# Performance work log

Measured on AMD Instinct MI355X. Metric: run time of the kernel, lower is better.

The kernel has to match this reference:

```python
import jax, jax.numpy as jnp
import numpy as np

NUM_GROUPS = 64
TOPK = 8
BLOCK_M = 128
NUM_TOKENS = 8192
HIDDEN = 4096


def _build_perm(flat_ids_np, num_groups, block_m):
    """Single-pass histogram + stable sort + per-expert padding.

    Returns sorted_token_ids (int64, [total_padded]) and m_indices (int32,
    [total_padded]) exactly matching the torch per-expert loop semantics:
    each expert's slot list padded to a multiple of block_m by repeating its
    last slot (or zeros for empty experts).
    Output length is data-dependent, so this runs on host numpy (concrete
    values), mirroring the original module whose output shape is also
    data-dependent.
    """
    n = flat_ids_np.shape[0]
    order = np.argsort(flat_ids_np, kind="stable")  # token slots grouped by expert
    counts = np.bincount(flat_ids_np, minlength=num_groups)
    padded = (counts + block_m - 1) // block_m * block_m
    in_starts = np.concatenate([[0], np.cumsum(counts)])
    out_starts = np.concatenate([[0], np.cumsum(padded)])
    total = int(out_starts[-1])
    sorted_token_ids = np.zeros(total, dtype=np.int64)
    m_indices = np.zeros(total, dtype=np.int32)
    for e in range(num_groups):  # fixed small expert count
        c, p, o = int(counts[e]), int(padded[e]), int(out_starts[e])
        m_indices[o:o + p] = e
        if c > 0:
            seg = order[int(in_starts[e]):int(in_starts[e]) + c]
            sorted_token_ids[o:o + c] = seg
            sorted_token_ids[o + c:o + p] = seg[-1]  # pad with last slot
        # empty expert: rows stay zero (matches torch.zeros branch)
    np.clip(sorted_token_ids, None, n - 1, out=sorted_token_ids)
    return sorted_token_ids, m_indices


def setup_inputs() -> dict:
    key = jax.random.key(0)
    k1, k2 = jax.random.split(key)
    hidden_states = jax.random.normal(k1, (NUM_TOKENS, HIDDEN), dtype=jnp.bfloat16)
    topk_ids = jax.random.randint(k2, (NUM_TOKENS, TOPK), 0, NUM_GROUPS, dtype=jnp.int32)
    return {"hidden_states": hidden_states, "topk_ids": topk_ids}


def reference(hidden_states, topk_ids):
    m, _ = hidden_states.shape
    num_flat = m * TOPK
    flat_ids = np.asarray(topk_ids).reshape(-1)
    sorted_token_ids_np, m_indices_np = _build_perm(flat_ids, NUM_GROUPS, BLOCK_M)
    sorted_token_ids = jnp.asarray(sorted_token_ids_np)
    m_indices = jnp.asarray(m_indices_np)
    # inverse permutation for later unpermute (stable argsort breaks pad ties deterministically)
    inv_perm = jnp.argsort(sorted_token_ids, stable=True)[:num_flat]
    source_token_idx = sorted_token_ids // TOPK  # expert-contiguous gather indices
    output = hidden_states[source_token_idx]     # [total_padded, HIDDEN] bf16 gather
    return output, m_indices, inv_perm
```

## Files before the change

kernel.cpp:

```cpp
#include <hip/hip_runtime.h>
#include <hip/hip_bf16.h>

#define NG 64
#define TOPK 8
#define BM 128
#define NSLOT 65536
#define HID 4096
#define NTOK 8192


__global__ __launch_bounds__(64) void init_k(int* ws) {
    int t = threadIdx.x;
    if (t < NG) { ws[t] = 0; ws[NG + t] = -1; }
}

__global__ void hist_k(const int* __restrict__ ids, int* __restrict__ ws) {
    __shared__ int h[NG];
    __shared__ int lm[NG];
    int t = threadIdx.x;
    if (t < NG) { h[t] = 0; lm[t] = -1; }
    __syncthreads();
    for (int i = blockIdx.x * blockDim.x + t; i < NSLOT; i += gridDim.x * blockDim.x) {
        int e = ids[i] & (NG - 1);
        atomicAdd(&h[e], 1);
        atomicMax(&lm[e], i);
    }
    __syncthreads();
    if (t < NG) {
        if (h[t]) atomicAdd(&ws[t], h[t]);
        atomicMax(&ws[NG + t], lm[t]);
    }
}

__global__ void scan_k(int* ws) {
    if (threadIdx.x == 0) {
        int acc = 0;
        for (int e = 0; e < NG; e++) {
            int c = ws[e];
            int p = (c + BM - 1) / BM * BM;
            ws[2 * NG + e] = p;
            ws[3 * NG + e] = acc;
            acc += p;
        }
        ws[256] = acc;
    }
}

__global__ __launch_bounds__(64) void rank_k(const int* __restrict__ ids,
                                             const int* __restrict__ ws,
                                             unsigned short* __restrict__ rank,
                                             float* __restrict__ out) {
    int e = blockIdx.x;
    int lane = threadIdx.x;
    int c = ws[e];
    int p = ws[2 * NG + e];
    int o = ws[3 * NG + e];
    int total = ws[256];

    if (c > 0) {
        int base_r = 0;
        for (int chunk = 0; chunk < NSLOT; chunk += 512) {
            int id[8];
#pragma unroll
            for (int u = 0; u < 8; u++) id[u] = ids[chunk + u * 64 + lane];
#pragma unroll
            for (int u = 0; u < 8; u++) {
                unsigned long long m = __ballot(id[u] == e);
                if (id[u] == e)
                    rank[chunk + u * 64 + lane] =
                        (unsigned short)(base_r + __popcll(m & ((1ULL << lane) - 1ULL)));
                base_r += __popcll(m);
            }
        }
    }
    float* m_out = out + (size_t)total * HID;
    float fe = (float)e;
    for (int t2 = lane; t2 < p; t2 += 64) {
        int idx = o + t2;
        if (idx >= 0 && idx < total) m_out[idx] = fe;
    }
}

__global__ void inv_k(const int* __restrict__ ids,
                      const int* __restrict__ ws,
                      const unsigned short* __restrict__ rank,
                      float* __restrict__ out) {
    __shared__ int s_last[NG], s_pad[NG];
    int t = threadIdx.x;
    if (t < NG) {
        s_last[t] = ws[NG + t];
        s_pad[t] = ws[2 * NG + t] - ws[t];
    }
    __syncthreads();
    int total = ws[256];
    float* inv_out = out + (size_t)total * (HID + 1);
    int i = blockIdx.x * blockDim.x + t;
    if (i >= NSLOT) return;
    int e = ids[i] & (NG - 1);
    int pos = ws[3 * NG + e] + (int)rank[i];
    int base = i;
#pragma unroll
    for (int f = 0; f < NG; f++) {
        int l = s_last[f];
        base += (l >= 0 && l < i) ? s_pad[f] : 0;
    }
    if (base >= 0 && base < NSLOT) inv_out[base] = (float)pos;
    if (i == s_last[e]) {
        int oc = ws[3 * NG + e] + ws[e];
        int pd = s_pad[e];
        for (int j = 0; j < pd; j++) {
            int idx = base + 1 + j;
            if (idx < 0 || idx >= NSLOT) break;
            inv_out[idx] = (float)(oc + j);
        }
    }
}

__global__ __launch_bounds__(256) void copy_k(const __hip_bfloat16* __restrict__ hs,
                                              const int* __restrict__ ids,
                                              const int* __restrict__ ws,
                                              const unsigned short* __restrict__ rank,
                                              float* __restrict__ out) {
    int b = blockIdx.x;
    int total = ws[256];
    int srcslot, dst;
    if (b < NSLOT) {
        int e = ids[b] & (NG - 1);
        srcslot = b;
        dst = ws[3 * NG + e] + (int)rank[b];
    } else {
        int q = b - NSLOT;
        int e = q >> 7;
        int j = q & 127;
        int c = ws[e];
        int p = ws[2 * NG + e];
        if (c + j >= p) return;
        srcslot = ws[NG + e];
        dst = ws[3 * NG + e] + c + j;
    }
    if (dst < 0 || dst >= total) return;
    int src = srcslot / TOPK;
    if (src < 0 || src >= NTOK) return;
    const uint4* s = (const uint4*)(hs + (size_t)src * HID);
    uint4* d = (uint4*)(out + (size_t)dst * HID);
    int t = threadIdx.x;
#pragma unroll
    for (int half = 0; half < 2; half++) {
        int v = half * 256 + t;
        uint4 w = s[v];
        uint4 o1, o2;
        o1.x = w.x << 16; o1.y = w.x & 0xFFFF0000u;
        o1.z = w.y << 16; o1.w = w.y & 0xFFFF0000u;
        o2.x = w.z << 16; o2.y = w.z & 0xFFFF0000u;
        o2.z = w.w << 16; o2.w = w.w & 0xFFFF0000u;
        d[2 * v] = o1;
        d[2 * v + 1] = o2;
    }
}

extern "C" void kernel_launch(void* const* d_in, const int* in_sizes, int n_in,
                              void* d_out, int out_size, void* d_ws, size_t ws_size,
                              hipStream_t stream) {
    const __hip_bfloat16* hs = (const __hip_bfloat16*)d_in[0];
    const int* ids = (const int*)d_in[1];
    float* out = (float*)d_out;

    int* ws = (int*)d_ws;
    unsigned short* rank = (unsigned short*)(ws + 512);

    hipLaunchKernelGGL(init_k, dim3(1), dim3(64), 0, stream, ws);
    hipLaunchKernelGGL(hist_k, dim3(64), dim3(256), 0, stream, ids, ws);
    hipLaunchKernelGGL(scan_k, dim3(1), dim3(64), 0, stream, ws);
    hipLaunchKernelGGL(rank_k, dim3(NG), dim3(64), 0, stream, ids, ws, rank, out);
    hipLaunchKernelGGL(inv_k, dim3(NSLOT / 256), dim3(256), 0, stream, ids, ws, rank, out);
    hipLaunchKernelGGL(copy_k, dim3(NSLOT + NG * BM), dim3(256), 0, stream,
                       hs, ids, ws, rank, out);
}
```

Baseline: 357.1 us.

## Segment histogram and rank per block to parallelize ranking; nontemporal output stores

Replaces the global atomic histogram with per-segment counts stored in the workspace, which removes the init kernel. The scan kernel now also builds per-segment prefix offsets for each expert, so ranking can be split across 4096 waves (expert × segment) instead of 64 waves that each scan all 65536 slots. The gather copy now uses nontemporal stores for the large fp32 output. The ranking kernel was a serial bottleneck; the cost is a larger workspace and a scan kernel with serial per-expert loops.

```diff
diff --git a/kernel.cpp b/kernel.cpp
--- a/kernel.cpp
+++ b/kernel.cpp
@@ -7,110 +7,117 @@
 #define NSLOT 65536
 #define HID 4096
 #define NTOK 8192
+#define NSEG 64
+
+typedef unsigned int v4u __attribute__((ext_vector_type(4)));
 
 
-__global__ __launch_bounds__(64) void init_k(int* ws) {
-    int t = threadIdx.x;
-    if (t < NG) { ws[t] = 0; ws[NG + t] = -1; }
-}
-
-__global__ void hist_k(const int* __restrict__ ids, int* __restrict__ ws) {
-    __shared__ int h[NG];
-    __shared__ int lm[NG];
-    int t = threadIdx.x;
+__global__ __launch_bounds__(256) void hist_k(const int* __restrict__ ids,
+                                              int* __restrict__ ws) {
+    __shared__ int h[NG], lm[NG];
+    int t = threadIdx.x, b = blockIdx.x;
     if (t < NG) { h[t] = 0; lm[t] = -1; }
     __syncthreads();
-    for (int i = blockIdx.x * blockDim.x + t; i < NSLOT; i += gridDim.x * blockDim.x) {
-        int e = ids[i] & (NG - 1);
+    int base = b * 1024;
+    for (int i = t; i < 1024; i += 256) {
+        int e = ids[base + i] & (NG - 1);
         atomicAdd(&h[e], 1);
-        atomicMax(&lm[e], i);
+        atomicMax(&lm[e], base + i);
     }
     __syncthreads();
     if (t < NG) {
-        if (h[t]) atomicAdd(&ws[t], h[t]);
-        atomicMax(&ws[NG + t], lm[t]);
+        ws[320 + t * 64 + b] = h[t];
+        ws[4416 + t * 64 + b] = lm[t];
     }
 }
 
-__global__ void scan_k(int* ws) {
-    if (threadIdx.x == 0) {
+__global__ __launch_bounds__(64) void scan_k(int* __restrict__ ws) {
+    int e = threadIdx.x;
+    int c = 0, last = -1;
+    for (int b = 0; b < NSEG; b++) {
+        c += ws[320 + e * 64 + b];
+        int l = ws[4416 + e * 64 + b];
+        last = l > last ? l : last;
+    }
+    ws[64 + e] = c;
+    ws[128 + e] = (c + BM - 1) / BM * BM;
+    ws[192 + e] = last;
+    __syncthreads();
+    if (e == 0) {
         int acc = 0;
-        for (int e = 0; e < NG; e++) {
-            int c = ws[e];
-            int p = (c + BM - 1) / BM * BM;
-            ws[2 * NG + e] = p;
-            ws[3 * NG + e] = acc;
-            acc += p;
-        }
+        for (int f = 0; f < NG; f++) { ws[f] = acc; acc += ws[128 + f]; }
         ws[256] = acc;
+    }
+    __syncthreads();
+    int acc = ws[e] - ws[e];
+    for (int b = 0; b < NSEG; b++) {
+        int sc = ws[320 + e * 64 + b];
+        ws[320 + e * 64 + b] = acc;
+        acc += sc;
     }
 }
 
-__global__ __launch_bounds__(64) void rank_k(const int* __restrict__ ids,
-                                             const int* __restrict__ ws,
-                                             unsigned short* __restrict__ rank,
-                                             float* __restrict__ out) {
-    int e = blockIdx.x;
-    int lane = threadIdx.x;
-    int c = ws[e];
-    int p = ws[2 * NG + e];
-    int o = ws[3 * NG + e];
-    int total = ws[256];
-
-    if (c > 0) {
-        int base_r = 0;
-        for (int chunk = 0; chunk < NSLOT; chunk += 512) {
-            int id[8];
+__global__ __launch_bounds__(256) void rank_k(const int* __restrict__ ids,
+                                              const int* __restrict__ ws,
+                                              unsigned short* __restrict__ rank,
+                                              float* __restrict__ out) {
+    int wid = blockIdx.x * 4 + (threadIdx.x >> 6);
+    int lane = threadIdx.x & 63;
+    int e = wid >> 6;
+    int s = wid & (NSEG - 1);
+    int base_r = ws[320 + e * 64 + s];
+    int segbase = s * 1024;
 #pragma unroll
-            for (int u = 0; u < 8; u++) id[u] = ids[chunk + u * 64 + lane];
+    for (int c0 = 0; c0 < 1024; c0 += 512) {
+        int id[8];
 #pragma unroll
-            for (int u = 0; u < 8; u++) {
-                unsigned long long m = __ballot(id[u] == e);
-                if (id[u] == e)
-                    rank[chunk + u * 64 + lane] =
-                        (unsigned short)(base_r + __popcll(m & ((1ULL << lane) - 1ULL)));
-                base_r += __popcll(m);
-            }
+        for (int u = 0; u < 8; u++) id[u] = ids[segbase + c0 + u * 64 + lane];
+#pragma unroll
+        for (int u = 0; u < 8; u++) {
+            unsigned long long m = __ballot(id[u] == e);
+            if (id[u] == e)
+                rank[segbase + c0 + u * 64 + lane] =
+                    (unsigned short)(base_r + __popcll(m & ((1ULL << lane) - 1ULL)));
+            base_r += __popcll(m);
         }
     }
-    float* m_out = out + (size_t)total * HID;
-    float fe = (float)e;
-    for (int t2 = lane; t2 < p; t2 += 64) {
-        int idx = o + t2;
-        if (idx >= 0 && idx < total) m_out[idx] = fe;
+    if (s == 0) {
+        int o = ws[e], p = ws[128 + e], total = ws[256];
+        float* m_out = out + (size_t)total * HID;
+        float fe = (float)e;
+        for (int t2 = lane; t2 < p; t2 += 64) m_out[o + t2] = fe;
     }
 }
 
-__global__ void inv_k(const int* __restrict__ ids,
-                      const int* __restrict__ ws,
-                      const unsigned short* __restrict__ rank,
-                      float* __restrict__ out) {
+__global__ __launch_bounds__(256) void inv_k(const int* __restrict__ ids,
+                                             const int* __restrict__ ws,
+                                             const unsigned short* __restrict__ rank,
+                                             float* __restrict__ out) {
     __shared__ int s_last[NG], s_pad[NG];
     int t = threadIdx.x;
     if (t < NG) {
-        s_last[t] = ws[NG + t];
-        s_pad[t] = ws[2 * NG + t] - ws[t];
+        s_last[t] = ws[192 + t];
+        s_pad[t] = ws[128 + t] - ws[64 + t];
     }
     __syncthreads();
     int total = ws[256];
     float* inv_out = out + (size_t)total * (HID + 1);
-    int i = blockIdx.x * blockDim.x + t;
-    if (i >= NSLOT) return;
+    int i = blockIdx.x * 256 + t;
     int e = ids[i] & (NG - 1);
-    int pos = ws[3 * NG + e] + (int)rank[i];
+    int pos = ws[e] + (int)rank[i];
     int base = i;
 #pragma unroll
     for (int f = 0; f < NG; f++) {
         int l = s_last[f];
         base += (l >= 0 && l < i) ? s_pad[f] : 0;
     }
-    if (base >= 0 && base < NSLOT) inv_out[base] = (float)pos;
+    if (base < NSLOT) inv_out[base] = (float)pos;
     if (i == s_last[e]) {
-        int oc = ws[3 * NG + e] + ws[e];
+        int oc = ws[e] + ws[64 + e];
         int pd = s_pad[e];
         for (int j = 0; j < pd; j++) {
             int idx = base + 1 + j;
-            if (idx < 0 || idx >= NSLOT) break;
+            if (idx >= NSLOT) break;
             inv_out[idx] = (float)(oc + j);
         }
     }
@@ -127,34 +134,30 @@
     if (b < NSLOT) {
         int e = ids[b] & (NG - 1);
         srcslot = b;
-        dst = ws[3 * NG + e] + (int)rank[b];
+        dst = ws[e] + (int)rank[b];
     } else {
         int q = b - NSLOT;
         int e = q >> 7;
         int j = q & 127;
-        int c = ws[e];
-        int p = ws[2 * NG + e];
+        int c = ws[64 + e], p = ws[128 + e];
         if (c + j >= p) return;
-        srcslot = ws[NG + e];
-        dst = ws[3 * NG + e] + c + j;
+        srcslot = ws[192 + e];
+        dst = ws[e] + c + j;
     }
     if (dst < 0 || dst >= total) return;
-    int src = srcslot / TOPK;
+    int src = srcslot >> 3;
     if (src < 0 || src >= NTOK) return;
-    const uint4* s = (const uint4*)(hs + (size_t)src * HID);
-    uint4* d = (uint4*)(out + (size_t)dst * HID);
+    const v4u* s = (const v4u*)(hs + (size_t)src * HID);
+    v4u* d = (v4u*)(out + (size_t)dst * HID);
     int t = threadIdx.x;
 #pragma unroll
     for (int half = 0; half < 2; half++) {
         int v = half * 256 + t;
-        uint4 w = s[v];
-        uint4 o1, o2;
-        o1.x = w.x << 16; o1.y = w.x & 0xFFFF0000u;
-        o1.z = w.y << 16; o1.w = w.y & 0xFFFF0000u;
-        o2.x = w.z << 16; o2.y = w.z & 0xFFFF0000u;
-        o2.z = w.w << 16; o2.w = w.w & 0xFFFF0000u;
-        d[2 * v] = o1;
-        d[2 * v + 1] = o2;
+        v4u w = s[v];
+        v4u o1 = {w.x << 16, w.x & 0xFFFF0000u, w.y << 16, w.y & 0xFFFF0000u};
+        v4u o2 = {w.z << 16, w.z & 0xFFFF0000u, w.w << 16, w.w & 0xFFFF0000u};
+        __builtin_nontemporal_store(o1, d + 2 * v);
+        __builtin_nontemporal_store(o2, d + 2 * v + 1);
     }
 }
 
@@ -166,12 +169,11 @@
     float* out = (float*)d_out;
 
     int* ws = (int*)d_ws;
-    unsigned short* rank = (unsigned short*)(ws + 512);
+    unsigned short* rank = (unsigned short*)(ws + 8704);
 
-    hipLaunchKernelGGL(init_k, dim3(1), dim3(64), 0, stream, ws);
-    hipLaunchKernelGGL(hist_k, dim3(64), dim3(256), 0, stream, ids, ws);
+    hipLaunchKernelGGL(hist_k, dim3(NSEG), dim3(256), 0, stream, ids, ws);
     hipLaunchKernelGGL(scan_k, dim3(1), dim3(64), 0, stream, ws);
-    hipLaunchKernelGGL(rank_k, dim3(NG), dim3(64), 0, stream, ids, ws, rank, out);
+    hipLaunchKernelGGL(rank_k, dim3(NG * NSEG / 4), dim3(256), 0, stream, ids, ws, rank, out);
     hipLaunchKernelGGL(inv_k, dim3(NSLOT / 256), dim3(256), 0, stream, ids, ws, rank, out);
     hipLaunchKernelGGL(copy_k, dim3(NSLOT + NG * BM), dim3(256), 0, stream,
                        hs, ids, ws, rank, out);
```

Measured after the change: 517.9 us. 45.1% more time.
